# Optimization experiments

Measured on AMD Instinct MI355X. Metric: run time of the kernel, lower is better.

## Reference

```python
import jax, jax.numpy as jnp
import numpy as np

B, S, D, H = 2, 4096, 512, 8
HD = D // H  # head_dim = 64


def setup_inputs() -> dict:
    key = jax.random.key(0)
    ks = jax.random.split(key, 7)
    scale = 1.0 / np.sqrt(D)
    return {
        "x": jax.random.normal(ks[0], (B, S, D), dtype=jnp.float32),
        "Wq": jax.random.uniform(ks[1], (D, D), jnp.float32, -scale, scale),
        "bq": jax.random.uniform(ks[2], (D,), jnp.float32, -scale, scale),
        "Wk": jax.random.uniform(ks[3], (D, D), jnp.float32, -scale, scale),
        "bk": jax.random.uniform(ks[4], (D,), jnp.float32, -scale, scale),
        "Wv": jax.random.uniform(ks[5], (D, D), jnp.float32, -scale, scale),
        "bv": jax.random.uniform(ks[6], (D,), jnp.float32, -scale, scale),
    }


def reference(x, Wq, bq, Wk, bk, Wv, bv):
    # torch Linear: y = x @ W.T + b
    q = x @ Wq.T + bq  # [B,S,D]
    k = x @ Wk.T + bk
    v = x @ Wv.T + bv
    # split heads -> [B,H,S,HD]
    q = q.reshape(B, S, H, HD).transpose(0, 2, 1, 3)
    k = k.reshape(B, S, H, HD).transpose(0, 2, 1, 3)
    v = v.reshape(B, S, H, HD).transpose(0, 2, 1, 3)
    # NOTE: module scales by sqrt(pitch_dim), NOT sqrt(head_dim) -- keep faithful.
    scores = jnp.einsum("bhqd,bhkd->bhqk", q, k) / jnp.sqrt(jnp.float32(D))
    causal = jnp.tril(jnp.ones((S, S), dtype=bool))  # lower-tri incl. diag allowed
    scores = jnp.where(causal, scores, -jnp.inf)
    attn = jax.nn.softmax(scores, axis=-1)
    out = jnp.einsum("bhqk,bhkd->bhqd", attn, v)  # [B,H,S,HD]
    return out.transpose(0, 2, 1, 3).reshape(B, S, D)
```

## Files before the change

### kernel.cpp

```cpp
#include <hip/hip_runtime.h>
#include <hip/hip_bf16.h>
#include <math.h>

#define BB 2
#define SS 4096
#define DD 512
#define HH 8
#define HD 64
#define MSD (BB*SS*DD)
#define WSZ (DD*DD)

#define XOFF (4*(size_t)MSD)
#define WOFF (5*(size_t)MSD)
#define POFF (3*(size_t)MSD)

typedef __attribute__((ext_vector_type(8))) short bf16x8;
typedef __attribute__((ext_vector_type(4))) float f32x4;

__device__ __forceinline__ unsigned short f2bf(float f) {
    unsigned int u = __float_as_uint(f);
    u += 0x7fff + ((u >> 16) & 1);
    return (unsigned short)(u >> 16);
}
__device__ __forceinline__ unsigned int pk2bf(float a, float b) {
    __hip_bfloat162 h = __float22bfloat162_rn(make_float2(a, b));
    union { __hip_bfloat162 h2; unsigned int u; } cv; cv.h2 = h;
    return cv.u;
}

#define GLD16(gsrc, ldst) \
    __builtin_amdgcn_global_load_lds((const __attribute__((address_space(1))) unsigned int*)(gsrc), \
                                     (__attribute__((address_space(3))) unsigned int*)(ldst), 16, 0, 0)

__global__ __launch_bounds__(256)
void convert_bf16(const float* __restrict__ x,
                  const float* __restrict__ Wq, const float* __restrict__ Wk,
                  const float* __restrict__ Wv, unsigned short* __restrict__ ws) {
    const int i8 = blockIdx.x*256 + threadIdx.x;
    const float* src; unsigned short* dst; size_t off;
    if (i8 < MSD/8) {
        src = x; dst = ws + XOFF; off = (size_t)i8 * 8;
    } else {
        size_t o = ((size_t)i8 - MSD/8) * 8;
        int wsel = (int)(o / WSZ);
        src = (wsel == 0) ? Wq : (wsel == 1) ? Wk : Wv;
        dst = ws + WOFF + (size_t)wsel*WSZ;
        off = o % WSZ;
    }
    float4 a = *(const float4*)&src[off];
    float4 b = *(const float4*)&src[off+4];
    unsigned short r[8] = { f2bf(a.x), f2bf(a.y), f2bf(a.z), f2bf(a.w),
                            f2bf(b.x), f2bf(b.y), f2bf(b.z), f2bf(b.w) };
    *(bf16x8*)&dst[off] = *(const bf16x8*)r;
}

__global__ __launch_bounds__(256)
void qkv_mfma(const float* __restrict__ bq, const float* __restrict__ bk,
              const float* __restrict__ bv, unsigned short* __restrict__ ws) {
    const int z = blockIdx.z;
    const unsigned short* Xb = ws + XOFF;
    const unsigned short* Wb = ws + WOFF + (size_t)z*WSZ;
    const float* bias = (z == 0) ? bq : (z == 1) ? bk : bv;
    unsigned short* dst = ws + (size_t)z*MSD;

    __shared__ __align__(16) unsigned short Sh[2*128*64];
    unsigned short* As = Sh;
    unsigned short* Bs = Sh + 128*64;

    const int tid  = threadIdx.x;
    const int w    = tid >> 6, l = tid & 63;
    const int quad = l >> 4,  r16 = l & 15;
    const int wy   = w >> 1,  wx  = w & 1;
    const int m0   = blockIdx.y * 128;
    const int n0   = blockIdx.x * 128;

    const int srow   = l >> 3;
    const int schunk = (l & 7) ^ srow;

    f32x4 acc[4][4];
    #pragma unroll
    for (int i = 0; i < 4; ++i)
        #pragma unroll
        for (int j = 0; j < 4; ++j) acc[i][j] = (f32x4){0.f,0.f,0.f,0.f};

    for (int k0 = 0; k0 < DD; k0 += 64) {
        __syncthreads();
        #pragma unroll
        for (int u = 0; u < 4; ++u) {
            const int r0 = w*32 + u*8;
            GLD16(&Xb[(size_t)(m0 + r0 + srow)*DD + k0 + schunk*8], &As[r0*64]);
            GLD16(&Wb[(size_t)(n0 + r0 + srow)*DD + k0 + schunk*8], &Bs[r0*64]);
        }
        __syncthreads();
        #pragma unroll
        for (int kc = 0; kc < 2; ++kc) {
            bf16x8 a[4], b[4];
            #pragma unroll
            for (int i = 0; i < 4; ++i) {
                const int mr = wy*64 + i*16 + r16;
                a[i] = *(const bf16x8*)&As[mr*64 + (((kc*4+quad) ^ (mr&7))*8)];
                const int nr = wx*64 + i*16 + r16;
                b[i] = *(const bf16x8*)&Bs[nr*64 + (((kc*4+quad) ^ (nr&7))*8)];
            }
            #pragma unroll
            for (int i = 0; i < 4; ++i)
                #pragma unroll
                for (int j = 0; j < 4; ++j) {
                    if (z == 2)
                        acc[i][j] = __builtin_amdgcn_mfma_f32_16x16x32_bf16(a[i], b[j], acc[i][j], 0, 0, 0);
                    else
                        acc[i][j] = __builtin_amdgcn_mfma_f32_16x16x32_bf16(b[j], a[i], acc[i][j], 0, 0, 0);
                }
        }
    }

    __syncthreads();

    const float qscale = 0.04419417382415922f * 1.4426950408889634f;
    if (z == 2) {
        #pragma unroll
        for (int j = 0; j < 4; ++j) {
            const int nloc = wx*64 + j*16 + r16;
            const float bz = bias[n0 + nloc];
            #pragma unroll
            for (int i = 0; i < 4; ++i) {
                const int chunk = wy*8 + i*2 + (quad>>1);
                const int off   = (quad & 1) * 4;
                unsigned short r4[4];
                #pragma unroll
                for (int reg = 0; reg < 4; ++reg)
                    r4[reg] = f2bf(acc[i][j][reg] + bz);
                *(uint2*)&Sh[nloc*128 + ((chunk ^ (nloc & 7))*8) + off] = *(const uint2*)r4;
            }
        }
    } else {
        #pragma unroll
        for (int j = 0; j < 4; ++j) {
            const int nbase = wx*64 + j*16 + quad*4;
            const float4 bz4 = *(const float4*)&bias[n0 + nbase];
            const int chunk = wx*8 + j*2 + (quad>>1);
            const int off   = (quad & 1) * 4;
            #pragma unroll
            for (int i = 0; i < 4; ++i) {
                const int mloc = wy*64 + i*16 + r16;
                float v0 = acc[i][j][0] + bz4.x;
                float v1 = acc[i][j][1] + bz4.y;
                float v2 = acc[i][j][2] + bz4.z;
                float v3 = acc[i][j][3] + bz4.w;
                if (z == 0) { v0 *= qscale; v1 *= qscale; v2 *= qscale; v3 *= qscale; }
                unsigned short r4[4] = { f2bf(v0), f2bf(v1), f2bf(v2), f2bf(v3) };
                *(uint2*)&Sh[mloc*128 + ((chunk ^ (mloc & 7))*8) + off] = *(const uint2*)r4;
            }
        }
    }
    __syncthreads();

    if (z == 2) {
        const int b_ = m0 >> 12, s0_ = m0 & (SS-1);
        #pragma unroll
        for (int p = 0; p < 8; ++p) {
            const int f = p*256 + tid;
            const int nrow = f >> 4;
            const int mch  = f & 15;
            bf16x8 v = *(const bf16x8*)&Sh[nrow*128 + ((mch ^ (nrow & 7))*8)];
            const int ng = n0 + nrow;
            const int h = ng >> 6, hd = ng & 63;
            *(bf16x8*)&dst[((size_t)(b_*HH + h)*HD + hd)*SS + s0_ + mch*8] = v;
        }
    } else {
        #pragma unroll
        for (int p = 0; p < 8; ++p) {
            const int f = p*256 + tid;
            const int hh  = f >> 10;
            const int rem = f & 1023;
            const int sr  = rem >> 3;
            const int ch  = rem & 7;
            bf16x8 v = *(const bf16x8*)&Sh[sr*128 + (((hh*8 + ch) ^ (sr & 7))*8)];
            const int mg = m0 + sr;
            const int b_ = mg >> 12, s_ = mg & (SS-1);
            const int hg = (n0 >> 6) + hh;
            *(bf16x8*)&dst[((size_t)(b_*HH + hg)*SS + s_)*HD + ch*8] = v;
        }
    }
}

__global__ __launch_bounds__(256)
void attn_mfma(unsigned short* __restrict__ ws, float* __restrict__ out) {
    const int bx = blockIdx.x;
    const int bh = bx & 15;
    const int uu = bx >> 4;
    int qb, half, split, t0, t1;
    if (uu < 32) {
        qb = 31 - (uu >> 1); half = uu & 1; split = 1;
        t0 = half ? (qb + 1) : 0;
        t1 = half ? (2*qb + 2) : (qb + 1);
    } else {
        qb = 47 - uu; half = 0; split = 0;
        t0 = 0; t1 = 2*qb + 2;
    }

    const int tid  = threadIdx.x;
    const int w    = tid >> 6, l = tid & 63;
    const int quad = l >> 4,  r16 = l & 15;
    const int qlo  = qb*128 + w*32;
    const int tdiag = 2*qb + (w >> 1);
    const int qoff  = 32*(w & 1);

    const unsigned short* Qg  = ws;
    const unsigned short* Kg  = ws + (size_t)MSD;
    const unsigned short* Vtg = ws + 2*(size_t)MSD;

    __shared__ __align__(16) unsigned short Ks[2][64*64];
    __shared__ __align__(16) unsigned short Vs[2][64*64];
    __shared__ __align__(16) unsigned int   Ps[4][32*36];
    unsigned int* PsW = Ps[w];

    const size_t kbase = (size_t)bh*SS*HD;
    const size_t vbase = (size_t)bh*HD*SS;

    bf16x8 bqf[2][2];
    #pragma unroll
    for (int nt = 0; nt < 2; ++nt)
        #pragma unroll
        for (int kc = 0; kc < 2; ++kc)
            bqf[nt][kc] = *(const bf16x8*)&Qg[kbase + (size_t)(qlo + nt*16 + r16)*HD + kc*32 + quad*8];

    f32x4 od[4][2];
    #pragma unroll
    for (int mt = 0; mt < 4; ++mt)
        #pragma unroll
        for (int nt = 0; nt < 2; ++nt) od[mt][nt] = (f32x4){0.f,0.f,0.f,0.f};
    float lsum[2] = {0.f, 0.f};

    const int sr8 = l >> 3, sc = l & 7;

    {
        const int jb0 = t0*64;
        #pragma unroll
        for (int u = 0; u < 2; ++u) {
            const int row = w*16 + u*8 + sr8;
            const int c   = sc ^ (row & 7);
            GLD16(&Kg [kbase + (size_t)(jb0 + row)*HD + c*8], &Ks[0][(w*16 + u*8)*64]);
            GLD16(&Vtg[vbase + (size_t)row*SS + jb0 + c*8],   &Vs[0][(w*16 + u*8)*64]);
        }
    }

    for (int t = t0; t < t1; ++t) {
        __syncthreads();

        if (t + 1 < t1) {
            const int jb1 = (t + 1)*64;
            const int b1  = (t + 1 - t0) & 1;
            #pragma unroll
            for (int u = 0; u < 2; ++u) {
                const int row = w*16 + u*8 + sr8;
                const int c   = sc ^ (row & 7);
                GLD16(&Kg [kbase + (size_t)(jb1 + row)*HD + c*8], &Ks[b1][(w*16 + u*8)*64]);
                GLD16(&Vtg[vbase + (size_t)row*SS + jb1 + c*8],   &Vs[b1][(w*16 + u*8)*64]);
            }
        }

        if (t <= tdiag) {
            const int bc = (t - t0) & 1;
            const unsigned short* Kb = Ks[bc];
            const unsigned short* Vb = Vs[bc];

            f32x4 z[4][2];
            #pragma unroll
            for (int mt = 0; mt < 4; ++mt) {
                const int row = mt*16 + r16;
                bf16x8 ak0 = *(const bf16x8*)&Kb[row*64 + ((quad     ^ (row&7))*8)];
                bf16x8 ak1 = *(const bf16x8*)&Kb[row*64 + (((4+quad) ^ (row&7))*8)];
                #pragma unroll
                for (int nt = 0; nt < 2; ++nt) {
                    z[mt][nt] = __builtin_amdgcn_mfma_f32_16x16x32_bf16(ak0, bqf[nt][0],
                                    (f32x4){0.f,0.f,0.f,0.f}, 0, 0, 0);
                    z[mt][nt] = __builtin_amdgcn_mfma_f32_16x16x32_bf16(ak1, bqf[nt][1], z[mt][nt], 0, 0, 0);
                }
            }

            if (t == tdiag) {
                #pragma unroll
                for (int mt = 0; mt < 4; ++mt)
                    #pragma unroll
                    for (int nt = 0; nt < 2; ++nt)
                        #pragma unroll
                        for (int reg = 0; reg < 4; ++reg)
                            if (mt*16 + quad*4 + reg > qoff + nt*16 + r16)
                                z[mt][nt][reg] = -1e30f;
            }

            #pragma unroll
            for (int mt = 0; mt < 4; ++mt)
                #pragma unroll
                for (int nt = 0; nt < 2; ++nt) {
                    #pragma unroll
                    for (int reg = 0; reg < 4; ++reg) {
                        z[mt][nt][reg] = __builtin_amdgcn_exp2f(z[mt][nt][reg]);
                        lsum[nt] += z[mt][nt][reg];
                    }
                    uint2 pk;
                    pk.x = pk2bf(z[mt][nt][0], z[mt][nt][1]);
                    pk.y = pk2bf(z[mt][nt][2], z[mt][nt][3]);
                    *(uint2*)&PsW[(nt*16 + r16)*36 + mt*8 + quad*2] = pk;
                }

            asm volatile("s_waitcnt lgkmcnt(0)" ::: "memory");

            bf16x8 pf[2][2];
            #pragma unroll
            for (int nt = 0; nt < 2; ++nt)
                #pragma unroll
                for (int kc = 0; kc < 2; ++kc)
                    pf[nt][kc] = *(const bf16x8*)&PsW[(nt*16 + r16)*36 + kc*16 + quad*4];

            #pragma unroll
            for (int mt = 0; mt < 4; ++mt) {
                const int row = mt*16 + r16;
                bf16x8 av0 = *(const bf16x8*)&Vb[row*64 + ((quad     ^ (row&7))*8)];
                bf16x8 av1 = *(const bf16x8*)&Vb[row*64 + (((4+quad) ^ (row&7))*8)];
                #pragma unroll
                for (int nt = 0; nt < 2; ++nt) {
                    od[mt][nt] = __builtin_amdgcn_mfma_f32_16x16x32_bf16(av0, pf[nt][0], od[mt][nt], 0, 0, 0);
                    od[mt][nt] = __builtin_amdgcn_mfma_f32_16x16x32_bf16(av1, pf[nt][1], od[mt][nt], 0, 0, 0);
                }
            }
        }
    }

    #pragma unroll
    for (int nt = 0; nt < 2; ++nt) {
        lsum[nt] += __shfl_xor(lsum[nt], 16);
        lsum[nt] += __shfl_xor(lsum[nt], 32);
    }

    if (split) {
        const int p = 2*(bh*16 + (qb - 16)) + half;
        float* Op = (float*)(ws + POFF) + (size_t)p*(128*64);
        float* Lp = (float*)(ws + WOFF) + p*128;
        #pragma unroll
        for (int nt = 0; nt < 2; ++nt) {
            const int qloc = w*32 + nt*16 + r16;
            if (quad == 0) Lp[qloc] = lsum[nt];
            #pragma unroll
            for (int mt = 0; mt < 4; ++mt)
                *(f32x4*)&Op[(size_t)qloc*64 + mt*16 + quad*4] = od[mt][nt];
        }
    } else {
        const int b_ = bh >> 3, h = bh & 7;
        #pragma unroll
        for (int nt = 0; nt < 2; ++nt) {
            const float inv = 1.0f / lsum[nt];
            const int q = qlo + nt*16 + r16;
            float* op = out + ((size_t)(b_*SS + q))*DD + h*HD;
            #pragma unroll
            for (int mt = 0; mt < 4; ++mt) {
                float4 tt;
                tt.x = od[mt][nt][0]*inv; tt.y = od[mt][nt][1]*inv;
                tt.z = od[mt][nt][2]*inv; tt.w = od[mt][nt][3]*inv;
                *(float4*)&op[mt*16 + quad*4] = tt;
            }
        }
    }
}

__global__ __launch_bounds__(256)
void attn_combine(const unsigned short* __restrict__ ws, float* __restrict__ out) {
    const int i  = blockIdx.x*256 + threadIdx.x;
    const int d4 = i & 15;
    const int q  = (i >> 4) & 127;
    const int r  = i >> 11;
    const int bh = r >> 4, qb = 16 + (r & 15);

    const float* Opart = (const float*)(ws + POFF);
    const float* Lpart = (const float*)(ws + WOFF);

    const float4 a = *(const float4*)&Opart[((size_t)(2*r)*128 + q)*64 + d4*4];
    const float4 b = *(const float4*)&Opart[((size_t)(2*r + 1)*128 + q)*64 + d4*4];
    const float lt = Lpart[(2*r)*128 + q] + Lpart[(2*r + 1)*128 + q];
    const float inv = 1.0f / lt;

    const int qg = qb*128 + q;
    const int b_ = bh >> 3, h = bh & 7;
    float4 o;
    o.x = (a.x + b.x)*inv; o.y = (a.y + b.y)*inv;
    o.z = (a.z + b.z)*inv; o.w = (a.w + b.w)*inv;
    *(float4*)&out[((size_t)(b_*SS + qg))*DD + h*HD + d4*4] = o;
}

extern "C" void kernel_launch(void* const* d_in, const int* in_sizes, int n_in,
                              void* d_out, int out_size, void* d_ws, size_t ws_size,
                              hipStream_t stream) {
    const float* x  = (const float*)d_in[0];
    const float* Wq = (const float*)d_in[1];
    const float* bq = (const float*)d_in[2];
    const float* Wk = (const float*)d_in[3];
    const float* bk = (const float*)d_in[4];
    const float* Wv = (const float*)d_in[5];
    const float* bv = (const float*)d_in[6];
    float* out = (float*)d_out;
    unsigned short* ws = (unsigned short*)d_ws;

    const int nconv = (MSD/8 + 3*WSZ/8 + 255) / 256;
    convert_bf16<<<nconv, 256, 0, stream>>>(x, Wq, Wk, Wv, ws);

    dim3 ggrid(DD/128, (BB*SS)/128, 3);
    qkv_mfma<<<ggrid, 256, 0, stream>>>(bq, bk, bv, ws);

    attn_mfma<<<768, 256, 0, stream>>>(ws, out);
    attn_combine<<<2048, 256, 0, stream>>>(ws, out);
}
```

Before: 187.8 us.

## Balance attention work via precomputed schedule table, MFMA row sums, and setprio

Replaces the arithmetic block-to-work mapping with a constant table that assigns each block a query block and key-tile range, grouping chunks into triples so that per-slot work is roughly equal. The softmax denominator now comes from an extra MFMA against a vector of bf16 ones rather than scalar adds plus cross-lane shuffles, so the sum is taken over the bf16-rounded probabilities. s_setprio is raised around the MFMA sections to favour matrix issue across waves. This adds a constant-memory lookup and a small precision change in the normalizer, and it depends on the block count and ordering matching the table.

Measured after the change: 173.6 us. -7.6%, faster.

```diff
diff --git a/kernel.cpp b/kernel.cpp
--- a/kernel.cpp
+++ b/kernel.cpp
@@ -31,6 +31,26 @@
 #define GLD16(gsrc, ldst) \
     __builtin_amdgcn_global_load_lds((const __attribute__((address_space(1))) unsigned int*)(gsrc), \
                                      (__attribute__((address_space(3))) unsigned int*)(ldst), 16, 0, 0)
+
+#define CH(qb,t0,t1) ((unsigned)(qb) | ((unsigned)(t0)<<8) | ((unsigned)(t1)<<16))
+__device__ __constant__ unsigned int SCHED[48] = {
+  CH(31,0,32),  CH(31,32,64), CH(0,0,2),
+  CH(15,0,32),  CH(29,0,30),  CH(1,0,4),
+  CH(29,30,60), CH(14,0,30),  CH(2,0,6),
+  CH(28,0,29),  CH(28,29,58), CH(3,0,8),
+  CH(27,0,28),  CH(13,0,28),  CH(4,0,10),
+  CH(26,0,27),  CH(26,27,54), CH(5,0,12),
+  CH(25,0,26),  CH(12,0,26),  CH(6,0,14),
+  CH(24,0,25),  CH(24,25,50), CH(7,0,16),
+  CH(30,0,31),  CH(17,0,18),  CH(16,0,17),
+  CH(30,31,62), CH(17,18,36), CH(16,17,34),
+  CH(27,28,56), CH(19,0,20),  CH(8,0,18),
+  CH(25,26,52), CH(20,0,21),  CH(18,0,19),
+  CH(23,0,24),  CH(22,0,23),  CH(18,19,38),
+  CH(23,24,48), CH(21,0,22),  CH(19,20,40),
+  CH(11,0,24),  CH(21,22,44), CH(9,0,20),
+  CH(22,23,46), CH(10,0,22),  CH(20,21,42),
+};
 
 __global__ __launch_bounds__(256)
 void convert_bf16(const float* __restrict__ x,
@@ -187,17 +207,16 @@
 __global__ __launch_bounds__(256)
 void attn_mfma(unsigned short* __restrict__ ws, float* __restrict__ out) {
     const int bx = blockIdx.x;
-    const int bh = bx & 15;
-    const int uu = bx >> 4;
-    int qb, half, split, t0, t1;
-    if (uu < 32) {
-        qb = 31 - (uu >> 1); half = uu & 1; split = 1;
-        t0 = half ? (qb + 1) : 0;
-        t1 = half ? (2*qb + 2) : (qb + 1);
-    } else {
-        qb = 47 - uu; half = 0; split = 0;
-        t0 = 0; t1 = 2*qb + 2;
-    }
+    const int k_ = bx >> 8;
+    const int j_ = bx & 255;
+    const int bh = j_ & 15;
+    const int ti = j_ >> 4;
+    const unsigned int e = SCHED[ti*3 + k_];
+    const int qb = e & 255;
+    const int t0 = (e >> 8) & 255;
+    const int t1 = (e >> 16) & 255;
+    const int split = !(t0 == 0 && t1 == 2*qb + 2);
+    const int half  = (t0 != 0);
 
     const int tid  = threadIdx.x;
     const int w    = tid >> 6, l = tid & 63;
@@ -225,12 +244,16 @@
         for (int kc = 0; kc < 2; ++kc)
             bqf[nt][kc] = *(const bf16x8*)&Qg[kbase + (size_t)(qlo + nt*16 + r16)*HD + kc*32 + quad*8];
 
+    const f32x4 ZZ = (f32x4){0.f,0.f,0.f,0.f};
+    const unsigned short onep[8] = {0x3F80,0x3F80,0x3F80,0x3F80,0x3F80,0x3F80,0x3F80,0x3F80};
+    const bf16x8 ones8 = *(const bf16x8*)onep;
+
     f32x4 od[4][2];
     #pragma unroll
     for (int mt = 0; mt < 4; ++mt)
         #pragma unroll
-        for (int nt = 0; nt < 2; ++nt) od[mt][nt] = (f32x4){0.f,0.f,0.f,0.f};
-    float lsum[2] = {0.f, 0.f};
+        for (int nt = 0; nt < 2; ++nt) od[mt][nt] = ZZ;
+    f32x4 lacc[2] = {ZZ, ZZ};
 
     const int sr8 = l >> 3, sc = l & 7;
 
@@ -266,6 +289,7 @@
             const unsigned short* Vb = Vs[bc];
 
             f32x4 z[4][2];
+            __builtin_amdgcn_s_setprio(1);
             #pragma unroll
             for (int mt = 0; mt < 4; ++mt) {
                 const int row = mt*16 + r16;
@@ -273,11 +297,11 @@
                 bf16x8 ak1 = *(const bf16x8*)&Kb[row*64 + (((4+quad) ^ (row&7))*8)];
                 #pragma unroll
                 for (int nt = 0; nt < 2; ++nt) {
-                    z[mt][nt] = __builtin_amdgcn_mfma_f32_16x16x32_bf16(ak0, bqf[nt][0],
-                                    (f32x4){0.f,0.f,0.f,0.f}, 0, 0, 0);
+                    z[mt][nt] = __builtin_amdgcn_mfma_f32_16x16x32_bf16(ak0, bqf[nt][0], ZZ, 0, 0, 0);
                     z[mt][nt] = __builtin_amdgcn_mfma_f32_16x16x32_bf16(ak1, bqf[nt][1], z[mt][nt], 0, 0, 0);
                 }
             }
+            __builtin_amdgcn_s_setprio(0);
 
             if (t == tdiag) {
                 #pragma unroll
@@ -294,14 +318,11 @@
             for (int mt = 0; mt < 4; ++mt)
                 #pragma unroll
                 for (int nt = 0; nt < 2; ++nt) {
-                    #pragma unroll
-                    for (int reg = 0; reg < 4; ++reg) {
-                        z[mt][nt][reg] = __builtin_amdgcn_exp2f(z[mt][nt][reg]);
-                        lsum[nt] += z[mt][nt][reg];
-                    }
                     uint2 pk;
-                    pk.x = pk2bf(z[mt][nt][0], z[mt][nt][1]);
-                    pk.y = pk2bf(z[mt][nt][2], z[mt][nt][3]);
+                    pk.x = pk2bf(__builtin_amdgcn_exp2f(z[mt][nt][0]),
+                                 __builtin_amdgcn_exp2f(z[mt][nt][1]));
+                    pk.y = pk2bf(__builtin_amdgcn_exp2f(z[mt][nt][2]),
+                                 __builtin_amdgcn_exp2f(z[mt][nt][3]));
                     *(uint2*)&PsW[(nt*16 + r16)*36 + mt*8 + quad*2] = pk;
                 }
 
@@ -314,6 +335,12 @@
                 for (int kc = 0; kc < 2; ++kc)
                     pf[nt][kc] = *(const bf16x8*)&PsW[(nt*16 + r16)*36 + kc*16 + quad*4];
 
+            __builtin_amdgcn_s_setprio(1);
+            #pragma unroll
+            for (int nt = 0; nt < 2; ++nt) {
+                lacc[nt] = __builtin_amdgcn_mfma_f32_16x16x32_bf16(ones8, pf[nt][0], lacc[nt], 0, 0, 0);
+                lacc[nt] = __builtin_amdgcn_mfma_f32_16x16x32_bf16(ones8, pf[nt][1], lacc[nt], 0, 0, 0);
+            }
             #pragma unroll
             for (int mt = 0; mt < 4; ++mt) {
                 const int row = mt*16 + r16;
@@ -325,13 +352,8 @@
                     od[mt][nt] = __builtin_amdgcn_mfma_f32_16x16x32_bf16(av1, pf[nt][1], od[mt][nt], 0, 0, 0);
                 }
             }
-        }
-    }
-
-    #pragma unroll
-    for (int nt = 0; nt < 2; ++nt) {
-        lsum[nt] += __shfl_xor(lsum[nt], 16);
-        lsum[nt] += __shfl_xor(lsum[nt], 32);
+            __builtin_amdgcn_s_setprio(0);
+        }
     }
 
     if (split) {
@@ -341,7 +363,7 @@
         #pragma unroll
         for (int nt = 0; nt < 2; ++nt) {
             const int qloc = w*32 + nt*16 + r16;
-            if (quad == 0) Lp[qloc] = lsum[nt];
+            if (quad == 0) Lp[qloc] = lacc[nt][0];
             #pragma unroll
             for (int mt = 0; mt < 4; ++mt)
                 *(f32x4*)&Op[(size_t)qloc*64 + mt*16 + quad*4] = od[mt][nt];
@@ -350,7 +372,7 @@
         const int b_ = bh >> 3, h = bh & 7;
         #pragma unroll
         for (int nt = 0; nt < 2; ++nt) {
-            const float inv = 1.0f / lsum[nt];
+            const float inv = 1.0f / lacc[nt][0];
             const int q = qlo + nt*16 + r16;
             float* op = out + ((size_t)(b_*SS + q))*DD + h*HD;
             #pragma unroll
```
